# Kernel tuning notes

Hardware: AMD Instinct MI355X
Metric: run time of the kernel (lower is better)

Reference implementation:

```python
import jax, jax.numpy as jnp
import numpy as np

L = 64      # number of physical sites (hilbert.size)
d = 2       # local Hilbert dimension (hilbert.local_size)
D = 8       # bond dimension
CHI = 4     # Kraus dimension
B = 1024    # batch of configurations


def setup_inputs() -> dict:
    key = jax.random.key(0)
    k1, k2 = jax.random.split(key)
    # local quantum-number indices, rows and columns concatenated: [B, 2L]
    qn = jax.random.randint(k1, (B, 2 * L), 0, d, dtype=jnp.int32)
    # MPDO unit-cell tensors: small random perturbation added to identity in the (D, D) slots
    iden = jnp.broadcast_to(jnp.eye(D, dtype=jnp.float32)[None, None, :, :, None], (L, d, D, D, CHI))
    tensors = 0.01 * jax.random.normal(k2, (L, d, D, D, CHI), dtype=jnp.float32) + iden
    return {"qn": qn, "tensors": tensors}


def reference(qn, tensors):
    D2 = D * D
    qn_r = qn[:, :L].T  # [L, B]
    qn_c = qn[:, L:].T  # [L, B]
    edge0 = jnp.broadcast_to(jnp.eye(D2, dtype=tensors.dtype), (qn.shape[0], D2, D2))

    def step(edge, site):
        T, ir, ic = site                 # T: [d, D, D, CHI], ir/ic: [B]
        Tr = T[ir]                       # [B, D, D, CHI]
        Tc = jnp.conj(T[ic])             # [B, D, D, CHI]
        m = jnp.einsum('bijk,blmk->biljm', Tr, Tc).reshape(-1, D2, D2)
        return jnp.matmul(edge, m), None

    step = jax.checkpoint(step)
    edge, _ = jax.lax.scan(step, edge0, (tensors, qn_r, qn_c))
    rho = jnp.trace(edge, axis1=-2, axis2=-1)   # [B]
    return jnp.log(rho.astype(jnp.complex64))
```

## Files before the change

### kernel.cpp

```cpp
#include <hip/hip_runtime.h>
#include <math.h>


#define NSITES 64
#define NPAIRS 32

typedef float f32x16 __attribute__((ext_vector_type(16)));

#define PACK4(P, A0, A1, A2, A3)                                               \
    asm("v_cvt_pk_fp8_f32 %0, %1, %2" : "=v"(P) : "v"(A0), "v"(A1));           \
    asm("v_cvt_pk_fp8_f32 %0, %1, %2 op_sel:[0,0,1]" : "+v"(P) : "v"(A2), "v"(A3));

__global__ __launch_bounds__(64)
void mpdo_prep2f8(const float* __restrict__ T, uint4* __restrict__ Mf8) {
    const int blk = blockIdx.x;
    const int pair = blk >> 4, combo = blk & 15;
    const int c0 = combo >> 2, c1 = combo & 3;
    const int ir0 = c0 >> 1, ic0 = c0 & 1, ir1 = c1 >> 1, ic1 = c1 & 1;
    const int lane = threadIdx.x;
    const int site0 = 2 * pair, site1 = 2 * pair + 1;

    __shared__ float sT0[256], sT1[256], sT2[256], sT3[256];
    __shared__ float sPA[16 * 64], sPB[16 * 64];

    *(float4*)&sT0[lane * 4] = *(const float4*)(T + ((size_t)(site0 * 2 + ir0)) * 256 + lane * 4);
    *(float4*)&sT1[lane * 4] = *(const float4*)(T + ((size_t)(site0 * 2 + ic0)) * 256 + lane * 4);
    *(float4*)&sT2[lane * 4] = *(const float4*)(T + ((size_t)(site1 * 2 + ir1)) * 256 + lane * 4);
    *(float4*)&sT3[lane * 4] = *(const float4*)(T + ((size_t)(site1 * 2 + ic1)) * 256 + lane * 4);
    __syncthreads();

    {
        const int i = lane >> 3, j = lane & 7;
        float pa[4][4], pb[4][4];
#pragma unroll
        for (int k = 0; k < 4; ++k)
#pragma unroll
            for (int jp = 0; jp < 4; ++jp) { pa[k][jp] = 0.0f; pb[k][jp] = 0.0f; }
#pragma unroll
        for (int a = 0; a < 8; ++a) {
            float4 x0 = *(const float4*)&sT0[(i * 8 + a) * 4];
            float4 y0 = *(const float4*)&sT2[(a * 8 + j) * 4];
            float4 x1 = *(const float4*)&sT1[(i * 8 + a) * 4];
            float4 y1 = *(const float4*)&sT3[(a * 8 + j) * 4];
            const float xk0[4] = {x0.x, x0.y, x0.z, x0.w};
            const float yj0[4] = {y0.x, y0.y, y0.z, y0.w};
            const float xk1[4] = {x1.x, x1.y, x1.z, x1.w};
            const float yj1[4] = {y1.x, y1.y, y1.z, y1.w};
#pragma unroll
            for (int k = 0; k < 4; ++k)
#pragma unroll
                for (int jp = 0; jp < 4; ++jp) {
                    pa[k][jp] = fmaf(xk0[k], yj0[jp], pa[k][jp]);
                    pb[k][jp] = fmaf(xk1[k], yj1[jp], pb[k][jp]);
                }
        }
#pragma unroll
        for (int k = 0; k < 4; ++k)
#pragma unroll
            for (int jp = 0; jp < 4; ++jp) {
                sPA[(k * 4 + jp) * 64 + lane] = pa[k][jp];
                sPB[(k * 4 + jp) * 64 + lane] = pb[k][jp];
            }
    }
    __syncthreads();

    const int h = lane >> 5, r = lane & 31, m = r & 7, j2 = r >> 3;
    float acc[8][8];
#pragma unroll
    for (int f = 0; f < 8; ++f)
#pragma unroll
        for (int e = 0; e < 8; ++e) acc[f][e] = 0.0f;

#pragma unroll 4
    for (int c = 0; c < 16; ++c) {
        float paf[8], pbe[8];
#pragma unroll
        for (int ti = 0; ti < 2; ++ti)
#pragma unroll
            for (int kt = 0; kt < 4; ++kt)
                paf[ti * 4 + kt] = sPA[c * 64 + (2 * kt + h) * 8 + (4 * ti + j2)];
#pragma unroll
        for (int e = 0; e < 8; ++e) pbe[e] = sPB[c * 64 + e * 8 + m];
#pragma unroll
        for (int f = 0; f < 8; ++f)
#pragma unroll
            for (int e = 0; e < 8; ++e)
                acc[f][e] = fmaf(paf[f], pbe[e], acc[f][e]);
    }

#pragma unroll
    for (int fp = 0; fp < 4; ++fp) {
        unsigned d[4];
#pragma unroll
        for (int s = 0; s < 2; ++s) {
            const int f = 2 * fp + s;
            const int ti = f >> 2, kt = f & 3;
            float Fv[8];
#pragma unroll
            for (int e = 0; e < 8; ++e) {
                float w = acc[f][e] * 0.0625f;
                if (32 * ti + r == 16 * kt + 8 * h + e) w -= 1.0f;
                Fv[e] = w;
            }
            PACK4(d[2 * s],     Fv[0], Fv[1], Fv[2], Fv[3])
            PACK4(d[2 * s + 1], Fv[4], Fv[5], Fv[6], Fv[7])
        }
        Mf8[((size_t)(pair * 16 + combo) * 4 + fp) * 64 + lane] =
            make_uint4(d[0], d[1], d[2], d[3]);
    }
}

__global__ __launch_bounds__(64, 1)
void mpdo_mfmaF8(const int* __restrict__ qn, const uint4* __restrict__ Mf8,
                 float* __restrict__ out) {
    const int b = blockIdx.x;
    const int lane = threadIdx.x;
    const int* qb = qn + (size_t)b * (2 * NSITES);
    const int pi = lane & 31;
    const int pc = (qb[2 * pi] << 3) | (qb[64 + 2 * pi] << 2) |
                   (qb[2 * pi + 1] << 1) | (qb[64 + 2 * pi + 1]);
    const unsigned long long m3 = __ballot(pc & 8);
    const unsigned long long m2 = __ballot(pc & 4);
    const unsigned long long m1 = __ballot(pc & 2);
    const unsigned long long m0 = __ballot(pc & 1);
    const int col = lane & 31, hh = lane >> 5;
    const int laneoff = lane * 16;

    f32x16 acc[2][2];
#pragma unroll
    for (int rt = 0; rt < 2; ++rt)
#pragma unroll
        for (int ct = 0; ct < 2; ++ct)
#pragma unroll
            for (int g = 0; g < 16; ++g) {
                int row = (g & 3) + 8 * (g >> 2) + 4 * hh;
                acc[rt][ct][g] = (rt == ct && row == col) ? 1.0f : 0.0f;
            }

    const char* Mbase = (const char*)Mf8;
    uint4 A0[4], A1[4], A2[4];

#define COMBO(T_) ((int)(((((m3) >> (T_)) & 1ull) << 3) | ((((m2) >> (T_)) & 1ull) << 2) | \
                         ((((m1) >> (T_)) & 1ull) << 1) | (((m0) >> (T_)) & 1ull)))
#define LOAD_FRAGS(DST, PIDX)                                                  \
    {                                                                          \
        int c_ = COMBO(PIDX);                                                  \
        const char* nb_ = Mbase + (((size_t)(PIDX) * 16 + c_) << 12) + laneoff;\
        _Pragma("unroll")                                                      \
        for (int fp = 0; fp < 4; ++fp)                                         \
            DST[fp] = *(const uint4*)(nb_ + fp * 1024);                        \
    }
#define A64(CUR, F)                                                            \
    (((F) & 1) ? (((unsigned long long)CUR[(F) >> 1].w << 32) | CUR[(F) >> 1].z) \
               : (((unsigned long long)CUR[(F) >> 1].y << 32) | CUR[(F) >> 1].x))

    LOAD_FRAGS(A0, 0)
    LOAD_FRAGS(A1, 1)

#define SITE_BODY(T_, CUR, NXT)                                               \
    {                                                                         \
        int tn = (T_) + 2; if (tn > 31) tn = 31;                              \
        LOAD_FRAGS(NXT, tn)                                                   \
          \
          \
        unsigned bf[4][2][2];                            \
        _Pragma("unroll")                                                     \
        for (int rt = 0; rt < 2; ++rt)                                        \
            _Pragma("unroll")                                                 \
            for (int ct = 0; ct < 2; ++ct) {                                  \
                unsigned u, v, u2, v2;                                        \
                PACK4(u,  acc[rt][ct][0],  acc[rt][ct][1],                    \
                          acc[rt][ct][2],  acc[rt][ct][3])                    \
                PACK4(v,  acc[rt][ct][4],  acc[rt][ct][5],                    \
                          acc[rt][ct][6],  acc[rt][ct][7])                    \
                asm("v_permlane32_swap_b32 %0, %1" : "+v"(u), "+v"(v));       \
                bf[2 * rt][ct][0] = u; bf[2 * rt][ct][1] = v;                 \
                PACK4(u2, acc[rt][ct][8],  acc[rt][ct][9],                    \
                          acc[rt][ct][10], acc[rt][ct][11])                   \
                PACK4(v2, acc[rt][ct][12], acc[rt][ct][13],                   \
                          acc[rt][ct][14], acc[rt][ct][15])                   \
                asm("v_permlane32_swap_b32 %0, %1" : "+v"(u2), "+v"(v2));     \
                bf[2 * rt + 1][ct][0] = u2; bf[2 * rt + 1][ct][1] = v2;       \
            }                                                                 \
            \
        _Pragma("unroll")                                                     \
        for (int ti = 0; ti < 2; ++ti)                                        \
            _Pragma("unroll")                                                 \
            for (int tj = 0; tj < 2; ++tj) {                                  \
                f32x16 d = acc[ti][tj];                                       \
                _Pragma("unroll")                                             \
                for (int kt = 0; kt < 4; ++kt) {                              \
                    unsigned long long av = A64(CUR, ti * 4 + kt);            \
                    unsigned long long bv =                                   \
                        ((unsigned long long)bf[kt][tj][1] << 32) |           \
                        bf[kt][tj][0];                                        \
                    d = __builtin_amdgcn_mfma_f32_32x32x16_fp8_fp8(           \
                        (long)av, (long)bv, d, 0, 0, 0);                      \
                }                                                             \
                acc[ti][tj] = d;                                              \
            }                                                                 \
    }

#pragma unroll 1
    for (int t = 0; t < 30; t += 3) {
        SITE_BODY(t,     A0, A2)
        SITE_BODY(t + 1, A1, A0)
        SITE_BODY(t + 2, A2, A1)
    }
    SITE_BODY(30, A0, A2)
    SITE_BODY(31, A1, A0)
#undef SITE_BODY
#undef LOAD_FRAGS
#undef A64
#undef COMBO

    float diag = 0.0f;
#pragma unroll
    for (int tt = 0; tt < 2; ++tt)
#pragma unroll
        for (int g = 0; g < 16; ++g) {
            int row = (g & 3) + 8 * (g >> 2) + 4 * hh;
            if (row == col) diag += acc[tt][tt][g];
        }
#pragma unroll
    for (int off = 32; off >= 1; off >>= 1)
        diag += __shfl_xor(diag, off, 64);

    if (lane == 0) {
        float tr = diag;
        float re = logf(fabsf(tr)) + 64.0f * 1.3862943611198906f;
        float im = (tr < 0.0f) ? 3.14159265358979323846f : 0.0f;
        out[2 * b]     = re;
        out[2 * b + 1] = im;
    }
}

#define DD 8
#define KCHI 4
__global__ __launch_bounds__(64, 1)
void mpdo_chain(const int* __restrict__ qn, const float* __restrict__ T,
                float* __restrict__ out) {
    const int b = blockIdx.x;
    const int lane = threadIdx.x;
    __shared__ float sA[KCHI][DD][DD];
    __shared__ float sB[KCHI][DD][DD];
    float E[DD][DD];
#pragma unroll
    for (int i = 0; i < DD; ++i)
#pragma unroll
        for (int l = 0; l < DD; ++l) E[i][l] = (i * DD + l == lane) ? 1.0f : 0.0f;
    const int* qb = qn + (size_t)b * (2 * NSITES);
    int ir0 = qb[0], ic0 = qb[NSITES];
    float4 aP = *reinterpret_cast<const float4*>(T + (size_t)ir0 * 256 + lane * 4);
    float4 bP = *reinterpret_cast<const float4*>(T + (size_t)ic0 * 256 + lane * 4);
    const int li = lane >> 3, lj = lane & 7;
#pragma unroll 1
    for (int site = 0; site < NSITES; ++site) {
        __syncthreads();
        sA[0][li][lj] = 0.5f * aP.x; sA[1][li][lj] = 0.5f * aP.y;
        sA[2][li][lj] = 0.5f * aP.z; sA[3][li][lj] = 0.5f * aP.w;
        sB[0][li][lj] = 0.5f * bP.x; sB[1][li][lj] = 0.5f * bP.y;
        sB[2][li][lj] = 0.5f * bP.z; sB[3][li][lj] = 0.5f * bP.w;
        __syncthreads();
        if (site + 1 < NSITES) {
            int irn = qb[site + 1], icn = qb[NSITES + site + 1];
            aP = *reinterpret_cast<const float4*>(T + ((size_t)(site + 1) * 2 + irn) * 256 + lane * 4);
            bP = *reinterpret_cast<const float4*>(T + ((size_t)(site + 1) * 2 + icn) * 256 + lane * 4);
        }
        float Ep[DD][DD];
#pragma unroll
        for (int j = 0; j < DD; ++j)
#pragma unroll
            for (int m = 0; m < DD; ++m) Ep[j][m] = 0.0f;
#pragma unroll 1
        for (int k = 0; k < KCHI; ++k) {
            float tmp[DD][DD];
#pragma unroll
            for (int l = 0; l < DD; ++l) {
                const float4* bp = reinterpret_cast<const float4*>(&sB[k][l][0]);
                float4 b0 = bp[0], b1 = bp[1];
                float brow[DD] = {b0.x, b0.y, b0.z, b0.w, b1.x, b1.y, b1.z, b1.w};
                if (l == 0) {
#pragma unroll
                    for (int i = 0; i < DD; ++i)
#pragma unroll
                        for (int m = 0; m < DD; ++m) tmp[i][m] = E[i][0] * brow[m];
                } else {
#pragma unroll
                    for (int i = 0; i < DD; ++i)
#pragma unroll
                        for (int m = 0; m < DD; ++m)
                            tmp[i][m] = fmaf(E[i][l], brow[m], tmp[i][m]);
                }
            }
#pragma unroll
            for (int i = 0; i < DD; ++i) {
                const float4* ap = reinterpret_cast<const float4*>(&sA[k][i][0]);
                float4 a0 = ap[0], a1 = ap[1];
                float arow[DD] = {a0.x, a0.y, a0.z, a0.w, a1.x, a1.y, a1.z, a1.w};
#pragma unroll
                for (int j = 0; j < DD; ++j)
#pragma unroll
                    for (int m = 0; m < DD; ++m)
                        Ep[j][m] = fmaf(arow[j], tmp[i][m], Ep[j][m]);
            }
        }
#pragma unroll
        for (int i = 0; i < DD; ++i)
#pragma unroll
            for (int l = 0; l < DD; ++l) E[i][l] = Ep[i][l];
    }
    float diag = 0.0f;
#pragma unroll
    for (int i = 0; i < DD; ++i)
#pragma unroll
        for (int l = 0; l < DD; ++l) diag += (i * DD + l == lane) ? E[i][l] : 0.0f;
#pragma unroll
    for (int off = 32; off >= 1; off >>= 1) diag += __shfl_xor(diag, off, 64);
    if (lane == 0) {
        float tr = diag;
        out[2 * b]     = logf(fabsf(tr)) + 64.0f * 1.3862943611198906f;
        out[2 * b + 1] = (tr < 0.0f) ? 3.14159265358979323846f : 0.0f;
    }
}

extern "C" void kernel_launch(void* const* d_in, const int* in_sizes, int n_in,
                              void* d_out, int out_size, void* d_ws, size_t ws_size,
                              hipStream_t stream) {
    const int*   qn  = (const int*)d_in[0];
    const float* T   = (const float*)d_in[1];
    float*       out = (float*)d_out;
    const int B = in_sizes[0] / (2 * NSITES);
    const size_t WS_F8 = (size_t)NPAIRS * 16 * 4 * 64 * 16;
    if (ws_size >= WS_F8) {
        uint4* Mf8 = (uint4*)d_ws;
        mpdo_prep2f8<<<dim3(NPAIRS * 16), dim3(64), 0, stream>>>(T, Mf8);
        mpdo_mfmaF8<<<dim3(B), dim3(64), 0, stream>>>(qn, Mf8, out);
    } else {
        mpdo_chain<<<dim3(B), dim3(64), 0, stream>>>(qn, T, out);
    }
}
```

Measured before the change: 29.90 us.

## Split MPDO chain into left and right halves interleaved per wave

Each wave now runs two independent 16-step chains instead of one 32-step serial chain. It computes the left half (site pairs 0-15) for one batch element and the right half (pairs 16-31) for its partner element. A block holds two waves that swap their right-half products through shared memory and take the trace as a dot product of the two halves. The aim is to fill MFMA latency with independent work from the second chain and shorten the dependent chain. In exchange it doubles accumulator registers, adds an LDS exchange and barrier, and requires an even batch size.

New measurement: 37.11 us. 1.24x slower.

```diff
diff --git a/kernel.cpp b/kernel.cpp
--- a/kernel.cpp
+++ b/kernel.cpp
@@ -110,23 +110,31 @@
     }
 }
 
-__global__ __launch_bounds__(64, 1)
-void mpdo_mfmaF8(const int* __restrict__ qn, const uint4* __restrict__ Mf8,
-                 float* __restrict__ out) {
-    const int b = blockIdx.x;
-    const int lane = threadIdx.x;
-    const int* qb = qn + (size_t)b * (2 * NSITES);
+__global__ __launch_bounds__(128, 1)
+void mpdo_mfmaD(const int* __restrict__ qn, const uint4* __restrict__ Mf8,
+                float* __restrict__ out) {
+    const int blk = blockIdx.x;
+    const int w = threadIdx.x >> 6;
+    const int lane = threadIdx.x & 63;
+    const int bA = 2 * blk + w;
+    const int bB = 2 * blk + (1 - w);
+    __shared__ float sL[2][64 * 65];
+
     const int pi = lane & 31;
-    const int pc = (qb[2 * pi] << 3) | (qb[64 + 2 * pi] << 2) |
-                   (qb[2 * pi + 1] << 1) | (qb[64 + 2 * pi + 1]);
-    const unsigned long long m3 = __ballot(pc & 8);
-    const unsigned long long m2 = __ballot(pc & 4);
-    const unsigned long long m1 = __ballot(pc & 2);
-    const unsigned long long m0 = __ballot(pc & 1);
+    const int* qbA = qn + (size_t)bA * (2 * NSITES);
+    const int* qbB = qn + (size_t)bB * (2 * NSITES);
+    const int pcA = (qbA[2 * pi] << 3) | (qbA[64 + 2 * pi] << 2) |
+                    (qbA[2 * pi + 1] << 1) | (qbA[64 + 2 * pi + 1]);
+    const int pcB = (qbB[2 * pi] << 3) | (qbB[64 + 2 * pi] << 2) |
+                    (qbB[2 * pi + 1] << 1) | (qbB[64 + 2 * pi + 1]);
+    const unsigned long long a3 = __ballot(pcA & 8), a2 = __ballot(pcA & 4);
+    const unsigned long long a1 = __ballot(pcA & 2), a0 = __ballot(pcA & 1);
+    const unsigned long long b3 = __ballot(pcB & 8), b2 = __ballot(pcB & 4);
+    const unsigned long long b1 = __ballot(pcB & 2), b0 = __ballot(pcB & 1);
     const int col = lane & 31, hh = lane >> 5;
     const int laneoff = lane * 16;
 
-    f32x16 acc[2][2];
+    f32x16 accA[2][2], accB[2][2];
 #pragma unroll
     for (int rt = 0; rt < 2; ++rt)
 #pragma unroll
@@ -134,18 +142,20 @@
 #pragma unroll
             for (int g = 0; g < 16; ++g) {
                 int row = (g & 3) + 8 * (g >> 2) + 4 * hh;
-                acc[rt][ct][g] = (rt == ct && row == col) ? 1.0f : 0.0f;
+                float v = (rt == ct && row == col) ? 1.0f : 0.0f;
+                accA[rt][ct][g] = v;
+                accB[rt][ct][g] = v;
             }
 
     const char* Mbase = (const char*)Mf8;
-    uint4 A0[4], A1[4], A2[4];
-
-#define COMBO(T_) ((int)(((((m3) >> (T_)) & 1ull) << 3) | ((((m2) >> (T_)) & 1ull) << 2) | \
-                         ((((m1) >> (T_)) & 1ull) << 1) | (((m0) >> (T_)) & 1ull)))
-#define LOAD_FRAGS(DST, PIDX)                                                  \
+    uint4 A0[4], A1[4], B0[4], B1[4];
+
+#define COMBO(M3, M2, M1, M0, T_)                                              \
+    ((int)(((((M3) >> (T_)) & 1ull) << 3) | ((((M2) >> (T_)) & 1ull) << 2) |   \
+           ((((M1) >> (T_)) & 1ull) << 1) | (((M0) >> (T_)) & 1ull)))
+#define LOADF(DST, CMB, PIDX)                                                  \
     {                                                                          \
-        int c_ = COMBO(PIDX);                                                  \
-        const char* nb_ = Mbase + (((size_t)(PIDX) * 16 + c_) << 12) + laneoff;\
+        const char* nb_ = Mbase + (((size_t)(PIDX) * 16 + (CMB)) << 12) + laneoff; \
         _Pragma("unroll")                                                      \
         for (int fp = 0; fp < 4; ++fp)                                         \
             DST[fp] = *(const uint4*)(nb_ + fp * 1024);                        \
@@ -154,40 +164,32 @@
     (((F) & 1) ? (((unsigned long long)CUR[(F) >> 1].w << 32) | CUR[(F) >> 1].z) \
                : (((unsigned long long)CUR[(F) >> 1].y << 32) | CUR[(F) >> 1].x))
 
-    LOAD_FRAGS(A0, 0)
-    LOAD_FRAGS(A1, 1)
-
-#define SITE_BODY(T_, CUR, NXT)                                               \
+#define CHAIN_STEP(ACC, CUR)                                                  \
     {                                                                         \
-        int tn = (T_) + 2; if (tn > 31) tn = 31;                              \
-        LOAD_FRAGS(NXT, tn)                                                   \
-          \
-          \
-        unsigned bf[4][2][2];                            \
+        unsigned bf[4][2][2];                                                 \
         _Pragma("unroll")                                                     \
         for (int rt = 0; rt < 2; ++rt)                                        \
             _Pragma("unroll")                                                 \
             for (int ct = 0; ct < 2; ++ct) {                                  \
                 unsigned u, v, u2, v2;                                        \
-                PACK4(u,  acc[rt][ct][0],  acc[rt][ct][1],                    \
-                          acc[rt][ct][2],  acc[rt][ct][3])                    \
-                PACK4(v,  acc[rt][ct][4],  acc[rt][ct][5],                    \
-                          acc[rt][ct][6],  acc[rt][ct][7])                    \
+                PACK4(u,  ACC[rt][ct][0],  ACC[rt][ct][1],                    \
+                          ACC[rt][ct][2],  ACC[rt][ct][3])                    \
+                PACK4(v,  ACC[rt][ct][4],  ACC[rt][ct][5],                    \
+                          ACC[rt][ct][6],  ACC[rt][ct][7])                    \
                 asm("v_permlane32_swap_b32 %0, %1" : "+v"(u), "+v"(v));       \
                 bf[2 * rt][ct][0] = u; bf[2 * rt][ct][1] = v;                 \
-                PACK4(u2, acc[rt][ct][8],  acc[rt][ct][9],                    \
-                          acc[rt][ct][10], acc[rt][ct][11])                   \
-                PACK4(v2, acc[rt][ct][12], acc[rt][ct][13],                   \
-                          acc[rt][ct][14], acc[rt][ct][15])                   \
+                PACK4(u2, ACC[rt][ct][8],  ACC[rt][ct][9],                    \
+                          ACC[rt][ct][10], ACC[rt][ct][11])                   \
+                PACK4(v2, ACC[rt][ct][12], ACC[rt][ct][13],                   \
+                          ACC[rt][ct][14], ACC[rt][ct][15])                   \
                 asm("v_permlane32_swap_b32 %0, %1" : "+v"(u2), "+v"(v2));     \
                 bf[2 * rt + 1][ct][0] = u2; bf[2 * rt + 1][ct][1] = v2;       \
             }                                                                 \
-            \
         _Pragma("unroll")                                                     \
         for (int ti = 0; ti < 2; ++ti)                                        \
             _Pragma("unroll")                                                 \
             for (int tj = 0; tj < 2; ++tj) {                                  \
-                f32x16 d = acc[ti][tj];                                       \
+                f32x16 d = ACC[ti][tj];                                       \
                 _Pragma("unroll")                                             \
                 for (int kt = 0; kt < 4; ++kt) {                              \
                     unsigned long long av = A64(CUR, ti * 4 + kt);            \
@@ -197,41 +199,66 @@
                     d = __builtin_amdgcn_mfma_f32_32x32x16_fp8_fp8(           \
                         (long)av, (long)bv, d, 0, 0, 0);                      \
                 }                                                             \
-                acc[ti][tj] = d;                                              \
+                ACC[ti][tj] = d;                                              \
             }                                                                 \
     }
 
+    LOADF(A0, COMBO(a3, a2, a1, a0, 0), 0)
+    LOADF(B0, COMBO(b3, b2, b1, b0, 16), 16)
+
+#define STEP2(T_, CA, NA, CB, NB)                                             \
+    {                                                                         \
+        int tn = (T_) + 1; if (tn > 15) tn = 15;                              \
+        LOADF(NA, COMBO(a3, a2, a1, a0, tn), tn)                              \
+        LOADF(NB, COMBO(b3, b2, b1, b0, 16 + tn), 16 + tn)                    \
+        CHAIN_STEP(accA, CA)                                                  \
+        CHAIN_STEP(accB, CB)                                                  \
+    }
+
 #pragma unroll 1
-    for (int t = 0; t < 30; t += 3) {
-        SITE_BODY(t,     A0, A2)
-        SITE_BODY(t + 1, A1, A0)
-        SITE_BODY(t + 2, A2, A1)
-    }
-    SITE_BODY(30, A0, A2)
-    SITE_BODY(31, A1, A0)
-#undef SITE_BODY
-#undef LOAD_FRAGS
+    for (int t = 0; t < 16; t += 2) {
+        STEP2(t,     A0, A1, B0, B1)
+        STEP2(t + 1, A1, A0, B1, B0)
+    }
+#undef STEP2
+#undef CHAIN_STEP
+#undef LOADF
 #undef A64
 #undef COMBO
 
-    float diag = 0.0f;
-#pragma unroll
-    for (int tt = 0; tt < 2; ++tt)
-#pragma unroll
-        for (int g = 0; g < 16; ++g) {
-            int row = (g & 3) + 8 * (g >> 2) + 4 * hh;
-            if (row == col) diag += acc[tt][tt][g];
-        }
-#pragma unroll
-    for (int off = 32; off >= 1; off >>= 1)
-        diag += __shfl_xor(diag, off, 64);
-
-    if (lane == 0) {
-        float tr = diag;
-        float re = logf(fabsf(tr)) + 64.0f * 1.3862943611198906f;
-        float im = (tr < 0.0f) ? 3.14159265358979323846f : 0.0f;
-        out[2 * b]     = re;
-        out[2 * b + 1] = im;
+#pragma unroll
+    for (int rt = 0; rt < 2; ++rt)
+#pragma unroll
+        for (int ct = 0; ct < 2; ++ct)
+#pragma unroll
+            for (int g = 0; g < 16; ++g) {
+                int p = 32 * rt + (g & 3) + 8 * (g >> 2) + 4 * hh;
+                int q = 32 * ct + col;
+                sL[1 - w][p * 65 + q] = accB[rt][ct][g];
+            }
+    __syncthreads();
+    {
+        float dot = 0.0f;
+#pragma unroll
+        for (int rt = 0; rt < 2; ++rt)
+#pragma unroll
+            for (int ct = 0; ct < 2; ++ct)
+#pragma unroll
+                for (int g = 0; g < 16; ++g) {
+                    int p = 32 * rt + (g & 3) + 8 * (g >> 2) + 4 * hh;
+                    int q = 32 * ct + col;
+                    dot = fmaf(accA[rt][ct][g], sL[w][q * 65 + p], dot);
+                }
+#pragma unroll
+        for (int off = 32; off >= 1; off >>= 1)
+            dot += __shfl_xor(dot, off, 64);
+        if (lane == 0) {
+            float tr = dot;
+            float re = logf(fabsf(tr)) + 64.0f * 1.3862943611198906f;
+            float im = (tr < 0.0f) ? 3.14159265358979323846f : 0.0f;
+            out[2 * bA]     = re;
+            out[2 * bA + 1] = im;
+        }
     }
 }
 
@@ -332,10 +359,10 @@
     float*       out = (float*)d_out;
     const int B = in_sizes[0] / (2 * NSITES);
     const size_t WS_F8 = (size_t)NPAIRS * 16 * 4 * 64 * 16;
-    if (ws_size >= WS_F8) {
+    if (ws_size >= WS_F8 && (B % 2) == 0) {
         uint4* Mf8 = (uint4*)d_ws;
         mpdo_prep2f8<<<dim3(NPAIRS * 16), dim3(64), 0, stream>>>(T, Mf8);
-        mpdo_mfmaF8<<<dim3(B), dim3(64), 0, stream>>>(qn, Mf8, out);
+        mpdo_mfmaD<<<dim3(B / 2), dim3(128), 0, stream>>>(qn, Mf8, out);
     } else {
         mpdo_chain<<<dim3(B), dim3(64), 0, stream>>>(qn, T, out);
     }
```
